# Optimization experiments

Hardware: AMD Instinct MI355X
Metric: run time of the kernel (lower is better)

Reference implementation:

```python
import jax, jax.numpy as jnp
import numpy as np


def setup_inputs() -> dict:
    key = jax.random.key(0)
    k1, k2, k3 = jax.random.split(key, 3)
    B, C, H, W = 8, 256, 64, 64
    l = jax.random.normal(k1, (B, C, H, W), dtype=jnp.float32)
    # 1x1 conv weights [out=C//2, in=C]; scale 1/sqrt(C) so projected features have ~unit variance
    scale = 1.0 / np.sqrt(C)
    w_theta = jax.random.normal(k2, (C // 2, C), dtype=jnp.float32) * scale
    w_phi = jax.random.normal(k3, (C // 2, C), dtype=jnp.float32) * scale
    return {"l": l, "w_theta": w_theta, "w_phi": w_phi}


def reference(l, w_theta, w_phi):
    # NonLocalOp forward with embed=True, softmax=True
    B, C, H, W = l.shape
    E = w_theta.shape[0]  # C // 2
    HW = H * W
    # 1x1 convs == per-pixel linear maps
    theta = jnp.einsum('bchw,ec->behw', l, w_theta).reshape(B, E, HW)  # [B,E,HW]
    phi = jnp.einsum('bchw,ec->behw', l, w_phi).reshape(B, E, HW)      # [B,E,HW]
    g = l.reshape(B, C, HW)                                            # [B,C,HW]
    # scores: theta^T phi over embed channels, scaled by sqrt(C//2)
    scale = 1.0 / jnp.sqrt(jnp.asarray(C // 2, dtype=l.dtype))
    f = jnp.einsum('beq,bek->bqk', theta, phi) * scale                 # [B,HW,HW]
    f = jax.nn.softmax(f, axis=-1)
    out = jnp.einsum('bqk,bck->bcq', f, g).reshape(B, C, H, W)
    return out
```

## Files before the change

### kernel.cpp

```cpp
#include <hip/hip_runtime.h>
#include <stdint.h>

#define NB 8
#define NC 256
#define NE 128
#define NHW 4096

typedef __bf16 v8bf __attribute__((ext_vector_type(8)));
typedef float v4f __attribute__((ext_vector_type(4)));
typedef float v16f __attribute__((ext_vector_type(16)));
typedef unsigned int v4u __attribute__((ext_vector_type(4)));

typedef unsigned int __attribute__((address_space(1))) uint_g;
typedef unsigned int __attribute__((address_space(3))) uint_l;

#if __has_builtin(__builtin_amdgcn_exp2f)
#define EXP2F(x) __builtin_amdgcn_exp2f(x)
#else
#define EXP2F(x) exp2f(x)
#endif

#define BARRIER_LDS() asm volatile("s_waitcnt lgkmcnt(0)\n\ts_barrier" ::: "memory")
#define WAIT_VM0()    asm volatile("s_waitcnt vmcnt(0)" ::: "memory")

__device__ __forceinline__ void dma16(const unsigned short* g, unsigned short* l) {
    __builtin_amdgcn_global_load_lds((const uint_g*)g, (uint_l*)l, 16, 0, 0);
}

__device__ __forceinline__ unsigned short f2bf(float x) {
    union { float f; unsigned int u; } v; v.f = x;
    unsigned int r = v.u + 0x7fffu + ((v.u >> 16) & 1u);
    return (unsigned short)(r >> 16);
}

__device__ __forceinline__ unsigned int pack_bf2_ru(float a, float b) {
    union { float f; unsigned int u; } va, vb; va.f = a; vb.f = b;
    return ((va.u + 0x8000u) >> 16) | ((vb.u + 0x8000u) & 0xffff0000u);
}

__global__ __launch_bounds__(256) void cast_w_kernel(const float* __restrict__ wt,
                                                     const float* __restrict__ wp,
                                                     unsigned short* __restrict__ Wbf) {
    int i = blockIdx.x * 256 + threadIdx.x;
    const float QS = 0.08838834764831845f * 1.4426950408889634f;
    float v = (i < 32768) ? wt[i] * QS : wp[i - 32768];
    Wbf[i] = f2bf(v);
}

__global__ __launch_bounds__(256, 2) void proj_kernel(const float* __restrict__ l,
                                                      const unsigned short* __restrict__ Wbf,
                                                      unsigned short* __restrict__ Qbf,
                                                      unsigned short* __restrict__ Kbf,
                                                      unsigned short* __restrict__ Vbf) {
    __shared__ __align__(16) unsigned short A[64][264];
    __shared__ __align__(16) unsigned short Ost[2][32][136];
    const int tid = threadIdx.x;
    const int b = blockIdx.x & 7;
    const int qt = (blockIdx.x >> 3) << 6;
    const float* lb = l + ((size_t)b * NC * NHW + qt);

    for (int s = 0; s < 16; ++s) {
        int f = tid + s * 256;
        int c = f >> 4, j = f & 15;
        float4 v = *(const float4*)(lb + (size_t)c * NHW + j * 4);
        ushort4 o4;
        o4.x = f2bf(v.x); o4.y = f2bf(v.y); o4.z = f2bf(v.z); o4.w = f2bf(v.w);
        A[j * 4 + 0][c] = o4.x;
        A[j * 4 + 1][c] = o4.y;
        A[j * 4 + 2][c] = o4.z;
        A[j * 4 + 3][c] = o4.w;
        *(ushort4*)(Vbf + (size_t)b * NC * NHW + (size_t)c * NHW + qt + j * 4) = o4;
    }
    __syncthreads();

    const int w = tid >> 6, L = tid & 63;
    const int l15 = L & 15, q4 = L >> 4;
    const v4f vz = {0.f, 0.f, 0.f, 0.f};
    v4f acc[4][4];
    for (int mt = 0; mt < 4; ++mt)
        for (int nt = 0; nt < 4; ++nt) acc[mt][nt] = vz;

    for (int kf = 0; kf < 8; ++kf) {
        int kc = kf * 32 + q4 * 8;
        v8bf a[4], bb[4];
        for (int mt = 0; mt < 4; ++mt)
            a[mt] = *(const v8bf*)&A[mt * 16 + l15][kc];
        for (int nt = 0; nt < 4; ++nt)
            bb[nt] = *(const v8bf*)(Wbf + (w * 64 + nt * 16 + l15) * 256 + kc);
        for (int mt = 0; mt < 4; ++mt)
            for (int nt = 0; nt < 4; ++nt)
                acc[mt][nt] = __builtin_amdgcn_mfma_f32_16x16x32_bf16(a[mt], bb[nt], acc[mt][nt], 0, 0, 0);
    }

    const int side = w >> 1;
    const int ebase = (w & 1) * 64;
#pragma unroll
    for (int ph = 0; ph < 2; ++ph) {
        __syncthreads();
#pragma unroll
        for (int mh = 0; mh < 2; ++mh) {
            int mt = ph * 2 + mh;
#pragma unroll
            for (int nt = 0; nt < 4; ++nt)
#pragma unroll
                for (int r = 0; r < 4; ++r) {
                    int q32 = mh * 16 + q4 * 4 + r;
                    Ost[side][q32][ebase + nt * 16 + l15] = f2bf(acc[mt][nt][r]);
                }
        }
        __syncthreads();
#pragma unroll
        for (int s = 0; s < 4; ++s) {
            int idx = tid + s * 256;
            int sd = idx >> 9, rem = idx & 511;
            int r32 = rem >> 4, c8 = rem & 15;
            unsigned short* dst = sd ? Kbf : Qbf;
            int c8s = sd ? (c8 ^ (r32 & 15)) : c8;
            *(uint4*)(dst + ((size_t)b * NHW + qt + ph * 32 + r32) * NE + c8s * 8) =
                *(const uint4*)&Ost[sd][r32][c8 * 8];
        }
    }
}

__global__ __launch_bounds__(512, 2) void attn_kernel(const unsigned short* __restrict__ Qbf,
                                                      const unsigned short* __restrict__ Kbf,
                                                      const unsigned short* __restrict__ Vbf,
                                                      float* __restrict__ out) {
    __shared__ __align__(16) unsigned char smem[66048];
    unsigned short* KuS = (unsigned short*)smem;
    unsigned short* PuS = (unsigned short*)(smem + 32768);
    float* lsumF = (float*)(smem + 65536);

    const int tid = threadIdx.x;
    const int b = blockIdx.x & 7;
    const int q128 = (blockIdx.x >> 3) << 7;
    const int w = tid >> 6;
    const int L = tid & 63;
    const int l31 = L & 31, hi = L >> 5;
    const int x15 = l31 & 15;

    const unsigned short* Kb = Kbf + (size_t)b * NHW * NE;
    const unsigned short* Vb = Vbf + (size_t)b * NC * NHW;

    v16f o[2][4];
#pragma unroll
    for (int ct = 0; ct < 2; ++ct)
#pragma unroll
        for (int qt = 0; qt < 4; ++qt)
#pragma unroll
            for (int r = 0; r < 16; ++r) o[ct][qt][r] = 0.f;
    float lacc = 0.f;

    v8bf bq[8];
    v8bf av[2][4];
    const unsigned short* vb0 = nullptr;
    const unsigned short* vb1 = nullptr;

    if (w < 4) {
        const unsigned short* qrow = Qbf + ((size_t)b * NHW + q128 + w * 32 + l31) * NE + hi * 8;
#pragma unroll
        for (int ef = 0; ef < 8; ++ef)
            bq[ef] = *(const v8bf*)(qrow + ef * 16);
#pragma unroll
        for (int jj = 0; jj < 4; ++jj) {
            int j = w * 4 + jj;
            dma16(Kb + (size_t)j * 512 + L * 8, KuS + j * 512);
        }
        WAIT_VM0();
    } else {
        int ci = w - 4;
        vb0 = Vb + (size_t)(ci * 64 + l31) * NHW + hi * 8;
        vb1 = Vb + (size_t)(ci * 64 + 32 + l31) * NHW + hi * 8;
#pragma unroll
        for (int kf = 0; kf < 4; ++kf) {
            av[0][kf] = *(const v8bf*)(vb0 + kf * 16);
            av[1][kf] = *(const v8bf*)(vb1 + kf * 16);
        }
    }
    BARRIER_LDS();

    for (int it = 0; it < 65; ++it) {
        if (w < 4 && it < 64) {
            const int buf = it & 1;
            const int nbuf = (it + 1) & 1;
            const size_t ktn = (size_t)((it + 1) & 63) * 64;
#pragma unroll
            for (int jj = 0; jj < 4; ++jj) {
                int j = w * 4 + jj;
                dma16(Kb + ktn * NE + (size_t)j * 512 + L * 8, KuS + nbuf * 8192 + j * 512);
            }
            const unsigned short* kub = KuS + buf * 8192;
#pragma unroll
            for (int kt = 0; kt < 2; ++kt) {
                v16f sa, sb;
#pragma unroll
                for (int r = 0; r < 16; ++r) { sa[r] = 0.f; sb[r] = 0.f; }
                const unsigned short* krow = kub + (kt * 32 + l31) * 128;
#pragma unroll
                for (int ef = 0; ef < 4; ++ef) {
                    v8bf ak0 = *(const v8bf*)(krow + (((2 * ef + hi) ^ x15) * 8));
                    v8bf ak1 = *(const v8bf*)(krow + (((2 * (ef + 4) + hi) ^ x15) * 8));
                    sa = __builtin_amdgcn_mfma_f32_32x32x16_bf16(ak0, bq[ef], sa, 0, 0, 0);
                    sb = __builtin_amdgcn_mfma_f32_32x32x16_bf16(ak1, bq[ef + 4], sb, 0, 0, 0);
                }
                float p[16];
#pragma unroll
                for (int r = 0; r < 16; ++r) p[r] = EXP2F(sa[r] + sb[r]);
#pragma unroll
                for (int r = 0; r < 16; ++r) lacc += p[r];
                unsigned int pk[8], px[8];
#pragma unroll
                for (int t = 0; t < 8; ++t) pk[t] = pack_bf2_ru(p[2 * t], p[2 * t + 1]);
#pragma unroll
                for (int t = 0; t < 8; ++t) px[t] = (unsigned int)__shfl_xor((int)pk[t], 32);
                union { v4u u; v8bf bb; } f0, f1;
                if (hi == 0) {
                    f0.u = (v4u){pk[0], pk[1], px[0], px[1]};
                    f1.u = (v4u){pk[4], pk[5], px[4], px[5]};
                } else {
                    f0.u = (v4u){px[2], px[3], pk[2], pk[3]};
                    f1.u = (v4u){px[6], px[7], pk[6], pk[7]};
                }
                unsigned short* pw_ = PuS + buf * 8192 + (w * 4 + kt * 2) * 512 + (hi * 32 + l31) * 8;
                *(v4u*)pw_ = f0.u;
                *(v4u*)(pw_ + 512) = f1.u;
            }
            WAIT_VM0();
        }
        if (w >= 4 && it > 0) {
            const int pbuf = (it - 1) & 1;
            const unsigned short* pb = PuS + pbuf * 8192 + (hi * 32 + l31) * 8;
#pragma unroll
            for (int qt = 0; qt < 4; ++qt) {
                v8bf bp[4];
#pragma unroll
                for (int kf = 0; kf < 4; ++kf)
                    bp[kf] = *(const v8bf*)(pb + (qt * 4 + kf) * 512);
#pragma unroll
                for (int kf = 0; kf < 4; ++kf) {
                    o[0][qt] = __builtin_amdgcn_mfma_f32_32x32x16_bf16(av[0][kf], bp[kf], o[0][qt], 0, 0, 0);
                    o[1][qt] = __builtin_amdgcn_mfma_f32_32x32x16_bf16(av[1][kf], bp[kf], o[1][qt], 0, 0, 0);
                }
            }
            const size_t kc0 = (size_t)(it & 63) * 64;
#pragma unroll
            for (int kf = 0; kf < 4; ++kf) {
                av[0][kf] = *(const v8bf*)(vb0 + kc0 + kf * 16);
                av[1][kf] = *(const v8bf*)(vb1 + kc0 + kf * 16);
            }
        }
        BARRIER_LDS();
    }

    if (w < 4) {
        float tot = lacc + __shfl_xor(lacc, 32);
        if (hi == 0) lsumF[w * 32 + l31] = tot;
    }
    BARRIER_LDS();
    if (w >= 4) {
        const int ci = w - 4;
        float inv[4];
#pragma unroll
        for (int qt = 0; qt < 4; ++qt) inv[qt] = 1.0f / lsumF[qt * 32 + l31];
#pragma unroll
        for (int ct = 0; ct < 2; ++ct)
#pragma unroll
            for (int qt = 0; qt < 4; ++qt) {
                float* ob = out + (size_t)b * NC * NHW + q128 + qt * 32 + l31;
#pragma unroll
                for (int r = 0; r < 16; ++r) {
                    int c = ci * 64 + ct * 32 + (r & 3) + 8 * (r >> 2) + 4 * hi;
                    ob[(size_t)c * NHW] = o[ct][qt][r] * inv[qt];
                }
            }
    }
}

extern "C" void kernel_launch(void* const* d_in, const int* in_sizes, int n_in,
                              void* d_out, int out_size, void* d_ws, size_t ws_size,
                              hipStream_t stream) {
    const float* l  = (const float*)d_in[0];
    const float* wt = (const float*)d_in[1];
    const float* wp = (const float*)d_in[2];
    float* out = (float*)d_out;

    char* ws = (char*)d_ws;
    unsigned short* Wbf = (unsigned short*)ws;
    unsigned short* Qbf = (unsigned short*)(ws + 131072);
    unsigned short* Kbf = (unsigned short*)(ws + 131072 + 8388608);
    unsigned short* Vbf = (unsigned short*)(ws + 131072 + 16777216);

    hipLaunchKernelGGL(cast_w_kernel, dim3(256), dim3(256), 0, stream, wt, wp, Wbf);
    hipLaunchKernelGGL(proj_kernel,   dim3(512), dim3(256), 0, stream, l, Wbf, Qbf, Kbf, Vbf);
    hipLaunchKernelGGL(attn_kernel,   dim3(256), dim3(512), 0, stream, Qbf, Kbf, Vbf, out);
}
```

Baseline: 216.0 us.

## Double attention block to 16 waves, splitting key subtiles and channel tiles

Doubles the attention block to 1024 threads: eight producer waves each compute scores for one 32-key half of a 64-key tile, and eight consumer waves each accumulate 32 output channels. Row sums from the two key halves are added before normalisation. The aim is more waves in flight per CU and fewer accumulator registers per wave, to hide MFMA and memory latency better. It adds barrier participants and duplicate Q register loads per block.

```diff
diff --git a/kernel.cpp b/kernel.cpp
--- a/kernel.cpp
+++ b/kernel.cpp
@@ -122,11 +122,11 @@
     }
 }
 
-__global__ __launch_bounds__(512, 2) void attn_kernel(const unsigned short* __restrict__ Qbf,
-                                                      const unsigned short* __restrict__ Kbf,
-                                                      const unsigned short* __restrict__ Vbf,
-                                                      float* __restrict__ out) {
-    __shared__ __align__(16) unsigned char smem[66048];
+__global__ __launch_bounds__(1024, 4) void attn_kernel(const unsigned short* __restrict__ Qbf,
+                                                       const unsigned short* __restrict__ Kbf,
+                                                       const unsigned short* __restrict__ Vbf,
+                                                       float* __restrict__ out) {
+    __shared__ __align__(16) unsigned char smem[66560];
     unsigned short* KuS = (unsigned short*)smem;
     unsigned short* PuS = (unsigned short*)(smem + 32768);
     float* lsumF = (float*)(smem + 65536);
@@ -138,96 +138,88 @@
     const int L = tid & 63;
     const int l31 = L & 31, hi = L >> 5;
     const int x15 = l31 & 15;
+    const int qsub = w & 3;
+    const int kth = (w >> 2) & 1;
+    const int ci = w - 8;
 
     const unsigned short* Kb = Kbf + (size_t)b * NHW * NE;
     const unsigned short* Vb = Vbf + (size_t)b * NC * NHW;
 
-    v16f o[2][4];
-#pragma unroll
-    for (int ct = 0; ct < 2; ++ct)
-#pragma unroll
-        for (int qt = 0; qt < 4; ++qt)
-#pragma unroll
-            for (int r = 0; r < 16; ++r) o[ct][qt][r] = 0.f;
+    v16f o[4];
     float lacc = 0.f;
-
     v8bf bq[8];
-    v8bf av[2][4];
+    v8bf av[4];
     const unsigned short* vb0 = nullptr;
-    const unsigned short* vb1 = nullptr;
-
-    if (w < 4) {
-        const unsigned short* qrow = Qbf + ((size_t)b * NHW + q128 + w * 32 + l31) * NE + hi * 8;
+
+    if (w < 8) {
+        const unsigned short* qrow = Qbf + ((size_t)b * NHW + q128 + qsub * 32 + l31) * NE + hi * 8;
 #pragma unroll
         for (int ef = 0; ef < 8; ++ef)
             bq[ef] = *(const v8bf*)(qrow + ef * 16);
 #pragma unroll
-        for (int jj = 0; jj < 4; ++jj) {
-            int j = w * 4 + jj;
+        for (int jj = 0; jj < 2; ++jj) {
+            int j = w * 2 + jj;
             dma16(Kb + (size_t)j * 512 + L * 8, KuS + j * 512);
         }
         WAIT_VM0();
     } else {
-        int ci = w - 4;
-        vb0 = Vb + (size_t)(ci * 64 + l31) * NHW + hi * 8;
-        vb1 = Vb + (size_t)(ci * 64 + 32 + l31) * NHW + hi * 8;
-#pragma unroll
-        for (int kf = 0; kf < 4; ++kf) {
-            av[0][kf] = *(const v8bf*)(vb0 + kf * 16);
-            av[1][kf] = *(const v8bf*)(vb1 + kf * 16);
-        }
+#pragma unroll
+        for (int qt = 0; qt < 4; ++qt)
+#pragma unroll
+            for (int r = 0; r < 16; ++r) o[qt][r] = 0.f;
+        vb0 = Vb + (size_t)(ci * 32 + l31) * NHW + hi * 8;
+#pragma unroll
+        for (int kf = 0; kf < 4; ++kf)
+            av[kf] = *(const v8bf*)(vb0 + kf * 16);
     }
     BARRIER_LDS();
 
     for (int it = 0; it < 65; ++it) {
-        if (w < 4 && it < 64) {
+        if (w < 8 && it < 64) {
             const int buf = it & 1;
             const int nbuf = (it + 1) & 1;
             const size_t ktn = (size_t)((it + 1) & 63) * 64;
 #pragma unroll
-            for (int jj = 0; jj < 4; ++jj) {
-                int j = w * 4 + jj;
+            for (int jj = 0; jj < 2; ++jj) {
+                int j = w * 2 + jj;
                 dma16(Kb + ktn * NE + (size_t)j * 512 + L * 8, KuS + nbuf * 8192 + j * 512);
             }
             const unsigned short* kub = KuS + buf * 8192;
-#pragma unroll
-            for (int kt = 0; kt < 2; ++kt) {
-                v16f sa, sb;
-#pragma unroll
-                for (int r = 0; r < 16; ++r) { sa[r] = 0.f; sb[r] = 0.f; }
-                const unsigned short* krow = kub + (kt * 32 + l31) * 128;
-#pragma unroll
-                for (int ef = 0; ef < 4; ++ef) {
-                    v8bf ak0 = *(const v8bf*)(krow + (((2 * ef + hi) ^ x15) * 8));
-                    v8bf ak1 = *(const v8bf*)(krow + (((2 * (ef + 4) + hi) ^ x15) * 8));
-                    sa = __builtin_amdgcn_mfma_f32_32x32x16_bf16(ak0, bq[ef], sa, 0, 0, 0);
-                    sb = __builtin_amdgcn_mfma_f32_32x32x16_bf16(ak1, bq[ef + 4], sb, 0, 0, 0);
-                }
-                float p[16];
-#pragma unroll
-                for (int r = 0; r < 16; ++r) p[r] = EXP2F(sa[r] + sb[r]);
-#pragma unroll
-                for (int r = 0; r < 16; ++r) lacc += p[r];
-                unsigned int pk[8], px[8];
-#pragma unroll
-                for (int t = 0; t < 8; ++t) pk[t] = pack_bf2_ru(p[2 * t], p[2 * t + 1]);
-#pragma unroll
-                for (int t = 0; t < 8; ++t) px[t] = (unsigned int)__shfl_xor((int)pk[t], 32);
-                union { v4u u; v8bf bb; } f0, f1;
-                if (hi == 0) {
-                    f0.u = (v4u){pk[0], pk[1], px[0], px[1]};
-                    f1.u = (v4u){pk[4], pk[5], px[4], px[5]};
-                } else {
-                    f0.u = (v4u){px[2], px[3], pk[2], pk[3]};
-                    f1.u = (v4u){px[6], px[7], pk[6], pk[7]};
-                }
-                unsigned short* pw_ = PuS + buf * 8192 + (w * 4 + kt * 2) * 512 + (hi * 32 + l31) * 8;
-                *(v4u*)pw_ = f0.u;
-                *(v4u*)(pw_ + 512) = f1.u;
-            }
+            v16f sa, sb;
+#pragma unroll
+            for (int r = 0; r < 16; ++r) { sa[r] = 0.f; sb[r] = 0.f; }
+            const unsigned short* krow = kub + (kth * 32 + l31) * 128;
+#pragma unroll
+            for (int ef = 0; ef < 4; ++ef) {
+                v8bf ak0 = *(const v8bf*)(krow + (((2 * ef + hi) ^ x15) * 8));
+                v8bf ak1 = *(const v8bf*)(krow + (((2 * (ef + 4) + hi) ^ x15) * 8));
+                sa = __builtin_amdgcn_mfma_f32_32x32x16_bf16(ak0, bq[ef], sa, 0, 0, 0);
+                sb = __builtin_amdgcn_mfma_f32_32x32x16_bf16(ak1, bq[ef + 4], sb, 0, 0, 0);
+            }
+            float p[16];
+#pragma unroll
+            for (int r = 0; r < 16; ++r) p[r] = EXP2F(sa[r] + sb[r]);
+#pragma unroll
+            for (int r = 0; r < 16; ++r) lacc += p[r];
+            unsigned int pk[8], px[8];
+#pragma unroll
+            for (int t = 0; t < 8; ++t) pk[t] = pack_bf2_ru(p[2 * t], p[2 * t + 1]);
+#pragma unroll
+            for (int t = 0; t < 8; ++t) px[t] = (unsigned int)__shfl_xor((int)pk[t], 32);
+            union { v4u u; v8bf bb; } f0, f1;
+            if (hi == 0) {
+                f0.u = (v4u){pk[0], pk[1], px[0], px[1]};
+                f1.u = (v4u){pk[4], pk[5], px[4], px[5]};
+            } else {
+                f0.u = (v4u){px[2], px[3], pk[2], pk[3]};
+                f1.u = (v4u){px[6], px[7], pk[6], pk[7]};
+            }
+            unsigned short* pw_ = PuS + buf * 8192 + (qsub * 4 + kth * 2) * 512 + (hi * 32 + l31) * 8;
+            *(v4u*)pw_ = f0.u;
+            *(v4u*)(pw_ + 512) = f1.u;
             WAIT_VM0();
         }
-        if (w >= 4 && it > 0) {
+        if (w >= 8 && it > 0) {
             const int pbuf = (it - 1) & 1;
             const unsigned short* pb = PuS + pbuf * 8192 + (hi * 32 + l31) * 8;
 #pragma unroll
@@ -237,42 +229,36 @@
                 for (int kf = 0; kf < 4; ++kf)
                     bp[kf] = *(const v8bf*)(pb + (qt * 4 + kf) * 512);
 #pragma unroll
-                for (int kf = 0; kf < 4; ++kf) {
-                    o[0][qt] = __builtin_amdgcn_mfma_f32_32x32x16_bf16(av[0][kf], bp[kf], o[0][qt], 0, 0, 0);
-                    o[1][qt] = __builtin_amdgcn_mfma_f32_32x32x16_bf16(av[1][kf], bp[kf], o[1][qt], 0, 0, 0);
-                }
+                for (int kf = 0; kf < 4; ++kf)
+                    o[qt] = __builtin_amdgcn_mfma_f32_32x32x16_bf16(av[kf], bp[kf], o[qt], 0, 0, 0);
             }
             const size_t kc0 = (size_t)(it & 63) * 64;
 #pragma unroll
-            for (int kf = 0; kf < 4; ++kf) {
-                av[0][kf] = *(const v8bf*)(vb0 + kc0 + kf * 16);
-                av[1][kf] = *(const v8bf*)(vb1 + kc0 + kf * 16);
-            }
+            for (int kf = 0; kf < 4; ++kf)
+                av[kf] = *(const v8bf*)(vb0 + kc0 + kf * 16);
         }
         BARRIER_LDS();
     }
 
-    if (w < 4) {
+    if (w < 8) {
         float tot = lacc + __shfl_xor(lacc, 32);
         if (hi == 0) lsumF[w * 32 + l31] = tot;
     }
     BARRIER_LDS();
-    if (w >= 4) {
-        const int ci = w - 4;
+    if (w >= 8) {
         float inv[4];
 #pragma unroll
-        for (int qt = 0; qt < 4; ++qt) inv[qt] = 1.0f / lsumF[qt * 32 + l31];
-#pragma unroll
-        for (int ct = 0; ct < 2; ++ct)
-#pragma unroll
-            for (int qt = 0; qt < 4; ++qt) {
-                float* ob = out + (size_t)b * NC * NHW + q128 + qt * 32 + l31;
-#pragma unroll
-                for (int r = 0; r < 16; ++r) {
-                    int c = ci * 64 + ct * 32 + (r & 3) + 8 * (r >> 2) + 4 * hi;
-                    ob[(size_t)c * NHW] = o[ct][qt][r] * inv[qt];
-                }
-            }
+        for (int qt = 0; qt < 4; ++qt)
+            inv[qt] = 1.0f / (lsumF[qt * 32 + l31] + lsumF[(qt + 4) * 32 + l31]);
+#pragma unroll
+        for (int qt = 0; qt < 4; ++qt) {
+            float* ob = out + (size_t)b * NC * NHW + q128 + qt * 32 + l31;
+#pragma unroll
+            for (int r = 0; r < 16; ++r) {
+                int c = ci * 32 + (r & 3) + 8 * (r >> 2) + 4 * hi;
+                ob[(size_t)c * NHW] = o[qt][r] * inv[qt];
+            }
+        }
     }
 }
 
@@ -292,5 +278,5 @@
 
     hipLaunchKernelGGL(cast_w_kernel, dim3(256), dim3(256), 0, stream, wt, wp, Wbf);
     hipLaunchKernelGGL(proj_kernel,   dim3(512), dim3(256), 0, stream, l, Wbf, Qbf, Kbf, Vbf);
-    hipLaunchKernelGGL(attn_kernel,   dim3(256), dim3(512), 0, stream, Qbf, Kbf, Vbf, out);
-}
+    hipLaunchKernelGGL(attn_kernel,   dim3(256), dim3(1024), 0, stream, Qbf, Kbf, Vbf, out);
+}
```

Result: slower. 366.8 us (+69.9%).

## Software-pipeline QK scores one tile ahead of softmax and add MFMA priority hints

Applied to the files above, without the earlier changes.

The QK^T score MFMAs for the next K tile now run in the same iteration as the exp/pack/store of the previous tile's scores. A prologue computes the first tile's scores, and the K prefetch moves two tiles ahead while reusing the double buffer. The aim is to let MFMA work overlap the transcendental and shuffle work in the score waves. s_setprio is raised around the MFMA blocks in both score and PV waves. This adds 32 live VGPRs of carried scores, which may raise register pressure and lower occupancy.

```diff
diff --git a/kernel.cpp b/kernel.cpp
--- a/kernel.cpp
+++ b/kernel.cpp
@@ -153,6 +153,7 @@
 
     v8bf bq[8];
     v8bf av[2][4];
+    v16f s_prev[2];
     const unsigned short* vb0 = nullptr;
     const unsigned short* vb1 = nullptr;
 
@@ -179,33 +180,71 @@
     }
     BARRIER_LDS();
 
+    if (w < 4) {
+#pragma unroll
+        for (int jj = 0; jj < 4; ++jj) {
+            int j = w * 4 + jj;
+            dma16(Kb + (size_t)64 * NE + (size_t)j * 512 + L * 8, KuS + 8192 + j * 512);
+        }
+        const unsigned short* kub = KuS;
+#pragma unroll
+        for (int kt = 0; kt < 2; ++kt) {
+            v16f sa, sb;
+#pragma unroll
+            for (int r = 0; r < 16; ++r) { sa[r] = 0.f; sb[r] = 0.f; }
+            const unsigned short* krow = kub + (kt * 32 + l31) * 128;
+#pragma unroll
+            for (int ef = 0; ef < 4; ++ef) {
+                v8bf ak0 = *(const v8bf*)(krow + (((2 * ef + hi) ^ x15) * 8));
+                v8bf ak1 = *(const v8bf*)(krow + (((2 * (ef + 4) + hi) ^ x15) * 8));
+                sa = __builtin_amdgcn_mfma_f32_32x32x16_bf16(ak0, bq[ef], sa, 0, 0, 0);
+                sb = __builtin_amdgcn_mfma_f32_32x32x16_bf16(ak1, bq[ef + 4], sb, 0, 0, 0);
+            }
+#pragma unroll
+            for (int r = 0; r < 16; ++r) s_prev[kt][r] = sa[r] + sb[r];
+        }
+        WAIT_VM0();
+    }
+    BARRIER_LDS();
+
     for (int it = 0; it < 65; ++it) {
         if (w < 4 && it < 64) {
             const int buf = it & 1;
-            const int nbuf = (it + 1) & 1;
-            const size_t ktn = (size_t)((it + 1) & 63) * 64;
-#pragma unroll
-            for (int jj = 0; jj < 4; ++jj) {
-                int j = w * 4 + jj;
-                dma16(Kb + ktn * NE + (size_t)j * 512 + L * 8, KuS + nbuf * 8192 + j * 512);
-            }
-            const unsigned short* kub = KuS + buf * 8192;
+            if (it <= 61) {
+                const size_t ktn = (size_t)(it + 2) * 64;
+#pragma unroll
+                for (int jj = 0; jj < 4; ++jj) {
+                    int j = w * 4 + jj;
+                    dma16(Kb + ktn * NE + (size_t)j * 512 + L * 8, KuS + buf * 8192 + j * 512);
+                }
+            }
+            v16f s_new[2];
+            if (it <= 62) {
+                const unsigned short* kub = KuS + ((it + 1) & 1) * 8192;
+                __builtin_amdgcn_s_setprio(1);
+#pragma unroll
+                for (int kt = 0; kt < 2; ++kt) {
+                    v16f sa, sb;
+#pragma unroll
+                    for (int r = 0; r < 16; ++r) { sa[r] = 0.f; sb[r] = 0.f; }
+                    const unsigned short* krow = kub + (kt * 32 + l31) * 128;
+#pragma unroll
+                    for (int ef = 0; ef < 4; ++ef) {
+                        v8bf ak0 = *(const v8bf*)(krow + (((2 * ef + hi) ^ x15) * 8));
+                        v8bf ak1 = *(const v8bf*)(krow + (((2 * (ef + 4) + hi) ^ x15) * 8));
+                        sa = __builtin_amdgcn_mfma_f32_32x32x16_bf16(ak0, bq[ef], sa, 0, 0, 0);
+                        sb = __builtin_amdgcn_mfma_f32_32x32x16_bf16(ak1, bq[ef + 4], sb, 0, 0, 0);
+                    }
+#pragma unroll
+                    for (int r = 0; r < 16; ++r) s_new[kt][r] = sa[r] + sb[r];
+                }
+                __builtin_amdgcn_s_setprio(0);
+            }
 #pragma unroll
             for (int kt = 0; kt < 2; ++kt) {
-                v16f sa, sb;
-#pragma unroll
-                for (int r = 0; r < 16; ++r) { sa[r] = 0.f; sb[r] = 0.f; }
-                const unsigned short* krow = kub + (kt * 32 + l31) * 128;
-#pragma unroll
-                for (int ef = 0; ef < 4; ++ef) {
-                    v8bf ak0 = *(const v8bf*)(krow + (((2 * ef + hi) ^ x15) * 8));
-                    v8bf ak1 = *(const v8bf*)(krow + (((2 * (ef + 4) + hi) ^ x15) * 8));
-                    sa = __builtin_amdgcn_mfma_f32_32x32x16_bf16(ak0, bq[ef], sa, 0, 0, 0);
-                    sb = __builtin_amdgcn_mfma_f32_32x32x16_bf16(ak1, bq[ef + 4], sb, 0, 0, 0);
-                }
                 float p[16];
 #pragma unroll
-                for (int r = 0; r < 16; ++r) p[r] = EXP2F(sa[r] + sb[r]);
+                for (int r = 0; r < 16; ++r) p[r] = EXP2F(s_prev[kt][r]);
 #pragma unroll
                 for (int r = 0; r < 16; ++r) lacc += p[r];
                 unsigned int pk[8], px[8];
@@ -225,11 +264,16 @@
                 *(v4u*)pw_ = f0.u;
                 *(v4u*)(pw_ + 512) = f1.u;
             }
+            if (it <= 62) {
+                s_prev[0] = s_new[0];
+                s_prev[1] = s_new[1];
+            }
             WAIT_VM0();
         }
         if (w >= 4 && it > 0) {
             const int pbuf = (it - 1) & 1;
             const unsigned short* pb = PuS + pbuf * 8192 + (hi * 32 + l31) * 8;
+            __builtin_amdgcn_s_setprio(1);
 #pragma unroll
             for (int qt = 0; qt < 4; ++qt) {
                 v8bf bp[4];
@@ -242,6 +286,7 @@
                     o[1][qt] = __builtin_amdgcn_mfma_f32_32x32x16_bf16(av[1][kf], bp[kf], o[1][qt], 0, 0, 0);
                 }
             }
+            __builtin_amdgcn_s_setprio(0);
             const size_t kc0 = (size_t)(it & 63) * 64;
 #pragma unroll
             for (int kf = 0; kf < 4; ++kf) {
```

Result: slower. 399.4 us (+84.9%).
